# Performance work log

Hardware: AMD Instinct MI355X
Metric: run time of the kernel (lower is better)

Reference implementation:

```python
import jax, jax.numpy as jnp
import numpy as np
from jax.scipy.special import logsumexp

# Module hyperparameters (init_kwargs)
K_TOP = 512
EPSILON = 0.1
MAX_ITER = 200
TOPK_ONLY = False

B, N = 512, 4096


def setup_inputs() -> dict:
    key = jax.random.key(0)
    scores = jax.random.normal(key, (B, N), dtype=jnp.float32)
    return {"scores": scores}


def _soft_topk_bottomk(scores, k=K_TOP, epsilon=EPSILON, max_iter=MAX_ITER,
                       topk_only=TOPK_ONLY):
    """SOFT (Sinkhorn/OT) differentiable top-k / top-k-bottom-k.

    Entropic-regularized optimal transport between the n scores (uniform
    source marginal) and a small set of anchor values. Output per element is
    n * (mass sent to the 'top' anchor) minus n * (mass sent to the 'bottom'
    anchor), giving ~+1 for soft top-k members, ~-1 for soft bottom-k members,
    ~0 otherwise (topk_only: just the soft top-k membership in [0,1]).
    """
    n = scores.shape[-1]
    dt = scores.dtype
    # Per-row min-max normalization to [0, 1] for numerical scale invariance.
    smin = jnp.min(scores, axis=-1, keepdims=True)
    smax = jnp.max(scores, axis=-1, keepdims=True)
    x = (scores - smin) / (smax - smin + jnp.asarray(1e-12, dt))

    if topk_only:
        anchors = jnp.array([0.0, 1.0], dtype=dt)               # [m]
        nu = jnp.array([(n - k) / n, k / n], dtype=dt)          # target marginal
    else:
        anchors = jnp.array([0.0, 0.5, 1.0], dtype=dt)
        nu = jnp.array([k / n, (n - 2 * k) / n, k / n], dtype=dt)

    m = anchors.shape[0]
    # Cost: squared distance between each score and each anchor. [B, n, m]
    C = (x[..., :, None] - anchors) ** 2
    Kmat = -C / jnp.asarray(epsilon, dt)      # Gibbs kernel in log space
    log_mu = -jnp.log(jnp.asarray(n, dt))     # uniform source marginal (scalar)
    log_nu = jnp.log(nu)                      # [m]

    batch_shape = x.shape[:-1]
    u0 = jnp.zeros(batch_shape + (n,), dt)    # scaled potential f/eps
    v0 = jnp.zeros(batch_shape + (m,), dt)    # scaled potential g/eps

    def step(carry, _):
        u, v = carry
        # row update: logsumexp over anchors (axis -1)
        u = log_mu - logsumexp(Kmat + v[..., None, :], axis=-1)
        # column update: logsumexp over the n scores (axis -2)
        v = log_nu - logsumexp(Kmat + u[..., :, None], axis=-2)
        return (u, v), None

    (u, v), _ = jax.lax.scan(step, (u0, v0), None, length=max_iter)

    # Transport plan Gamma[b, i, j] = exp(u_i + v_j - C_ij/eps)
    Gamma = jnp.exp(Kmat + u[..., :, None] + v[..., None, :])
    nf = jnp.asarray(n, dt)
    if topk_only:
        return Gamma[..., 1] * nf
    return (Gamma[..., 2] - Gamma[..., 0]) * nf


def reference(scores):
    return _soft_topk_bottomk(scores)
```

## Files before the change

### kernel.cpp

```cpp
#include <hip/hip_runtime.h>
#include <math.h>


constexpr int N_ELEM  = 4096;
constexpr int THREADS = 256;
constexpr int NWAVE   = THREADS / 64;
constexpr int HBINS   = 128;
constexpr int BPL     = HBINS / 64;
constexpr int MAXIT   = 200;

template<int CTRL>
__device__ __forceinline__ float dpp_add(float x) {
    int y = __builtin_amdgcn_update_dpp(0, __float_as_int(x), CTRL, 0xF, 0xF, true);
    return x + __int_as_float(y);
}
__device__ __forceinline__ float wave_sum63(float x) {
    x = dpp_add<0x111>(x);
    x = dpp_add<0x112>(x);
    x = dpp_add<0x114>(x);
    x = dpp_add<0x118>(x);
    x = dpp_add<0x142>(x);
    x = dpp_add<0x143>(x);
    return x;
}
__device__ __forceinline__ float bcast63(float x) {
    return __int_as_float(__builtin_amdgcn_readlane(__float_as_int(x), 63));
}
__device__ __forceinline__ float aitken(float a, float b, float c) {
    const float d2  = c - b, d1 = b - a;
    const float den = d2 - d1;
    float cand = c - d2 * d2 * __builtin_amdgcn_rcpf(den);
    cand = fminf(fmaxf(cand, 0.25f * c), 4.0f * c);
    return (fabsf(den) > 1e-6f * fabsf(d2) + 1e-18f) ? cand : c;
}

__global__ __launch_bounds__(THREADS)
void SoftTopKBottomK_kernel(const float* __restrict__ scores,
                            float* __restrict__ out)
{
    const int row  = blockIdx.x;
    const int t    = threadIdx.x;
    const int lane = t & 63;
    const int wave = t >> 6;

    const float4* srow = (const float4*)(scores + (size_t)row * N_ELEM);
    float4*       orow = (float4*)(out + (size_t)row * N_ELEM);

    __shared__ unsigned long long hb[NWAVE][HBINS];
    __shared__ float s_mm[NWAVE][2];

    for (int b = t; b < NWAVE * HBINS; b += THREADS) (&hb[0][0])[b] = 0ull;

    float4 xs[4];
    float lmin = INFINITY, lmax = -INFINITY;
#pragma unroll
    for (int c = 0; c < 4; ++c) {
        xs[c] = srow[c * THREADS + t];
        lmin = fminf(lmin, fminf(fminf(xs[c].x, xs[c].y), fminf(xs[c].z, xs[c].w)));
        lmax = fmaxf(lmax, fmaxf(fmaxf(xs[c].x, xs[c].y), fmaxf(xs[c].z, xs[c].w)));
    }
#pragma unroll
    for (int off = 32; off > 0; off >>= 1) {
        lmin = fminf(lmin, __shfl_xor(lmin, off, 64));
        lmax = fmaxf(lmax, __shfl_xor(lmax, off, 64));
    }
    if (lane == 0) { s_mm[wave][0] = lmin; s_mm[wave][1] = lmax; }
    __syncthreads();
    const float smin = fminf(fminf(s_mm[0][0], s_mm[1][0]), fminf(s_mm[2][0], s_mm[3][0]));
    const float smax = fmaxf(fmaxf(s_mm[0][1], s_mm[1][1]), fmaxf(s_mm[2][1], s_mm[3][1]));
    const float inv  = 1.0f / (smax - smin + 1e-12f);

#pragma unroll
    for (int c = 0; c < 4; ++c) {
        const float xv[4] = {xs[c].x, xs[c].y, xs[c].z, xs[c].w};
#pragma unroll
        for (int q = 0; q < 4; ++q) {
            const float x = (xv[q] - smin) * inv;
            int idx = (int)(x * (float)HBINS);
            idx = min(idx, HBINS - 1);
            const unsigned long long zfix =
                (unsigned long long)(unsigned int)(x * 655360.0f + 0.5f);
            atomicAdd(&hb[wave][idx], (1ull << 40) + zfix);
        }
    }
    __syncthreads();

    float cb[BPL], sb[BPL], rb[BPL], csb[BPL], crb[BPL];
#pragma unroll
    for (int j = 0; j < BPL; ++j) {
        const int b = lane + 64 * j;
        const unsigned long long u =
            ((hb[0][b] + hb[1][b]) + (hb[2][b] + hb[3][b]));
        const float c    = (float)(unsigned int)(u >> 40);
        const float zsum = (float)(u & 0xFFFFFFFFFFull);
        const float zbar = zsum * __builtin_amdgcn_rcpf(65536.0f * fmaxf(c, 1.0f)) - 5.0f;
        cb[j]  = c;
        sb[j]  = __expf(zbar);
        rb[j]  = __expf(-zbar);
        csb[j] = c * sb[j];
        crb[j] = c * rb[j];
    }

    const float Kc = 0.0820849986238988f;
    float e0 = Kc, e1 = 1.0f, e2 = Kc;
    float e0p = e0, e1p = e1, e2p = e2;
    float a0 = Kc, a1 = 1.0f, a2 = Kc, b0 = Kc, b1 = 1.0f, b2 = Kc;

    for (int it = 0; it < MAXIT; ++it) {
        float S0, S1, S2;
        {
            const float g0 = fmaf(rb[0], e0, fmaf(sb[0], e2, e1));
            const float g1 = fmaf(rb[1], e0, fmaf(sb[1], e2, e1));
            const float p0 = __builtin_amdgcn_rcpf(g0);
            const float p1 = __builtin_amdgcn_rcpf(g1);
            S1 = fmaf(cb[0],  p0, cb[1]  * p1);
            S0 = fmaf(crb[0], p0, crb[1] * p1);
            S2 = fmaf(csb[0], p0, csb[1] * p1);
        }
        S0 = bcast63(wave_sum63(S0));
        S1 = bcast63(wave_sum63(S1));
        S2 = bcast63(wave_sum63(S2));

        e0p = e0; e1p = e1; e2p = e2;
        e0 = 512.0f  * __builtin_amdgcn_rcpf(S0);
        e1 = 3072.0f * __builtin_amdgcn_rcpf(S1);
        e2 = 512.0f  * __builtin_amdgcn_rcpf(S2);

        const int ph = it & 7;
        if (ph == 5)      { a0 = e0; a1 = e1; a2 = e2; }
        else if (ph == 6) { b0 = e0; b1 = e1; b2 = e2; }
        else if (ph == 7) {
            e0 = aitken(a0, b0, e0);
            e1 = aitken(a1, b1, e1);
            e2 = aitken(a2, b2, e2);
        } else if (ph == 3) {
            const float d0 = fabsf(e0 - e0p) - 1e-5f * e0;
            const float d1 = fabsf(e1 - e1p) - 1e-5f * e1;
            const float d2 = fabsf(e2 - e2p) - 1e-5f * e2;
            if (fmaxf(fmaxf(d0, d1), d2) <= 0.0f) break;
        }
    }

#pragma unroll
    for (int c = 0; c < 4; ++c) {
        const float xv[4] = {xs[c].x, xs[c].y, xs[c].z, xs[c].w};
        float4 o;
        float* op = &o.x;
#pragma unroll
        for (int q = 0; q < 4; ++q) {
            const float x  = (xv[q] - smin) * inv;
            const float z  = 10.0f * x - 5.0f;
            const float s  = __expf(z);
            const float rs = __expf(-z);
            const float g  = fmaf(rs, e0p, fmaf(s, e2p, e1p));
            const float p  = __builtin_amdgcn_rcpf(g);
            op[q] = p * (s * e2 - rs * e0);
        }
        orow[c * THREADS + t] = o;
    }
}

extern "C" void kernel_launch(void* const* d_in, const int* in_sizes, int n_in,
                              void* d_out, int out_size, void* d_ws, size_t ws_size,
                              hipStream_t stream)
{
    const float* scores = (const float*)d_in[0];
    float* out = (float*)d_out;
    const int rows = in_sizes[0] / N_ELEM;
    SoftTopKBottomK_kernel<<<rows, THREADS, 0, stream>>>(scores, out);
}
```

Measured before the change: 64.05 us.

## Replace Sinkhorn fixed-point loop with fixed plain iterations plus 2D Newton solve

```diff
diff --git a/kernel.cpp b/kernel.cpp
--- a/kernel.cpp
+++ b/kernel.cpp
@@ -7,7 +7,8 @@
 constexpr int NWAVE   = THREADS / 64;
 constexpr int HBINS   = 128;
 constexpr int BPL     = HBINS / 64;
-constexpr int MAXIT   = 200;
+constexpr int N_PLAIN = 6;
+constexpr int N_NEWT  = 8;
 
 template<int CTRL>
 __device__ __forceinline__ float dpp_add(float x) {
@@ -25,13 +26,6 @@
 }
 __device__ __forceinline__ float bcast63(float x) {
     return __int_as_float(__builtin_amdgcn_readlane(__float_as_int(x), 63));
-}
-__device__ __forceinline__ float aitken(float a, float b, float c) {
-    const float d2  = c - b, d1 = b - a;
-    const float den = d2 - d1;
-    float cand = c - d2 * d2 * __builtin_amdgcn_rcpf(den);
-    cand = fminf(fmaxf(cand, 0.25f * c), 4.0f * c);
-    return (fabsf(den) > 1e-6f * fabsf(d2) + 1e-18f) ? cand : c;
 }
 
 __global__ __launch_bounds__(THREADS)
@@ -85,7 +79,7 @@
     }
     __syncthreads();
 
-    float cb[BPL], sb[BPL], rb[BPL], csb[BPL], crb[BPL];
+    float cb[BPL], sb[BPL], rb[BPL], crb[BPL], csb[BPL], crb2[BPL], csb2[BPL];
 #pragma unroll
     for (int j = 0; j < BPL; ++j) {
         const int b = lane + 64 * j;
@@ -94,51 +88,66 @@
         const float c    = (float)(unsigned int)(u >> 40);
         const float zsum = (float)(u & 0xFFFFFFFFFFull);
         const float zbar = zsum * __builtin_amdgcn_rcpf(65536.0f * fmaxf(c, 1.0f)) - 5.0f;
-        cb[j]  = c;
-        sb[j]  = __expf(zbar);
-        rb[j]  = __expf(-zbar);
-        csb[j] = c * sb[j];
-        crb[j] = c * rb[j];
+        cb[j]   = c;
+        sb[j]   = __expf(zbar);
+        rb[j]   = __expf(-zbar);
+        crb[j]  = c * rb[j];
+        csb[j]  = c * sb[j];
+        crb2[j] = crb[j] * rb[j];
+        csb2[j] = csb[j] * sb[j];
     }
 
     const float Kc = 0.0820849986238988f;
-    float e0 = Kc, e1 = 1.0f, e2 = Kc;
-    float e0p = e0, e1p = e1, e2p = e2;
-    float a0 = Kc, a1 = 1.0f, a2 = Kc, b0 = Kc, b1 = 1.0f, b2 = Kc;
+    float t0 = Kc, t2 = Kc;
+    for (int it = 0; it < N_PLAIN; ++it) {
+        float A = 0.f, B = 0.f, S1 = 0.f;
+#pragma unroll
+        for (int j = 0; j < BPL; ++j) {
+            const float g = fmaf(rb[j], t0, fmaf(sb[j], t2, 1.0f));
+            const float q = __builtin_amdgcn_rcpf(g);
+            S1 = fmaf(cb[j],  q, S1);
+            A  = fmaf(crb[j], q, A);
+            B  = fmaf(csb[j], q, B);
+        }
+        A  = bcast63(wave_sum63(A));
+        B  = bcast63(wave_sum63(B));
+        S1 = bcast63(wave_sum63(S1));
+        const float s6 = S1 * (1.0f / 6.0f);
+        t0 = s6 * __builtin_amdgcn_rcpf(A);
+        t2 = s6 * __builtin_amdgcn_rcpf(B);
+    }
 
-    for (int it = 0; it < MAXIT; ++it) {
-        float S0, S1, S2;
-        {
-            const float g0 = fmaf(rb[0], e0, fmaf(sb[0], e2, e1));
-            const float g1 = fmaf(rb[1], e0, fmaf(sb[1], e2, e1));
-            const float p0 = __builtin_amdgcn_rcpf(g0);
-            const float p1 = __builtin_amdgcn_rcpf(g1);
-            S1 = fmaf(cb[0],  p0, cb[1]  * p1);
-            S0 = fmaf(crb[0], p0, crb[1] * p1);
-            S2 = fmaf(csb[0], p0, csb[1] * p1);
+    for (int it = 0; it < N_NEWT; ++it) {
+        float A = 0.f, B = 0.f, P = 0.f, Q = 0.f, R = 0.f;
+#pragma unroll
+        for (int j = 0; j < BPL; ++j) {
+            const float g  = fmaf(rb[j], t0, fmaf(sb[j], t2, 1.0f));
+            const float q  = __builtin_amdgcn_rcpf(g);
+            const float q2 = q * q;
+            A = fmaf(crb[j],  q,  A);
+            B = fmaf(csb[j],  q,  B);
+            P = fmaf(cb[j],   q2, P);
+            Q = fmaf(crb2[j], q2, Q);
+            R = fmaf(csb2[j], q2, R);
         }
-        S0 = bcast63(wave_sum63(S0));
-        S1 = bcast63(wave_sum63(S1));
-        S2 = bcast63(wave_sum63(S2));
+        A = bcast63(wave_sum63(A));
+        B = bcast63(wave_sum63(B));
+        P = bcast63(wave_sum63(P));
+        Q = bcast63(wave_sum63(Q));
+        R = bcast63(wave_sum63(R));
 
-        e0p = e0; e1p = e1; e2p = e2;
-        e0 = 512.0f  * __builtin_amdgcn_rcpf(S0);
-        e1 = 3072.0f * __builtin_amdgcn_rcpf(S1);
-        e2 = 512.0f  * __builtin_amdgcn_rcpf(S2);
-
-        const int ph = it & 7;
-        if (ph == 5)      { a0 = e0; a1 = e1; a2 = e2; }
-        else if (ph == 6) { b0 = e0; b1 = e1; b2 = e2; }
-        else if (ph == 7) {
-            e0 = aitken(a0, b0, e0);
-            e1 = aitken(a1, b1, e1);
-            e2 = aitken(a2, b2, e2);
-        } else if (ph == 3) {
-            const float d0 = fabsf(e0 - e0p) - 1e-5f * e0;
-            const float d1 = fabsf(e1 - e1p) - 1e-5f * e1;
-            const float d2 = fabsf(e2 - e2p) - 1e-5f * e2;
-            if (fmaxf(fmaxf(d0, d1), d2) <= 0.0f) break;
-        }
+        const float G0  = fmaf(t0, A, -512.0f);
+        const float G2  = fmaf(t2, B, -512.0f);
+        const float J00 = fmaf(-t0, Q, A);
+        const float J11 = fmaf(-t2, R, B);
+        const float J01 = -t0 * P;
+        const float J10 = -t2 * P;
+        const float det = fmaf(J00, J11, -J01 * J10);
+        const float rdt = __builtin_amdgcn_rcpf(det);
+        const float d0  = -(J11 * G0 - J01 * G2) * rdt;
+        const float d2  = -(J00 * G2 - J10 * G0) * rdt;
+        t0 = fminf(fmaxf(t0 + d0, 0.125f * t0), 8.0f * t0);
+        t2 = fminf(fmaxf(t2 + d2, 0.125f * t2), 8.0f * t2);
     }
 
 #pragma unroll
@@ -147,14 +156,14 @@
         float4 o;
         float* op = &o.x;
 #pragma unroll
-        for (int q = 0; q < 4; ++q) {
-            const float x  = (xv[q] - smin) * inv;
+        for (int q4 = 0; q4 < 4; ++q4) {
+            const float x  = (xv[q4] - smin) * inv;
             const float z  = 10.0f * x - 5.0f;
             const float s  = __expf(z);
             const float rs = __expf(-z);
-            const float g  = fmaf(rs, e0p, fmaf(s, e2p, e1p));
-            const float p  = __builtin_amdgcn_rcpf(g);
-            op[q] = p * (s * e2 - rs * e0);
+            const float g  = fmaf(rs, t0, fmaf(s, t2, 1.0f));
+            const float q  = __builtin_amdgcn_rcpf(g);
+            op[q4] = q * (s * t2 - rs * t0);
         }
         orow[c * THREADS + t] = o;
     }
```

New measurement: 63.65 us. About the same (-0.6%).
